# Performance work log

Measured on AMD Instinct MI355X. Metric: run time of the kernel, lower is better.

## Reference

```python
import jax, jax.numpy as jnp
import numpy as np

N = 30000   # nodes
E = 240000  # edges
G = 16      # graphs in batch
DIMS = [1, 256, 512, 1024]
OUT = 1024

def _xavier(key, fan_in, fan_out):
    lim = float(np.sqrt(6.0 / (fan_in + fan_out)))
    return jax.random.uniform(key, (fan_in, fan_out), minval=-lim, maxval=lim, dtype=jnp.float32)

def setup_inputs() -> dict:
    key = jax.random.key(0)
    ks = jax.random.split(key, 8)
    x = jax.random.normal(ks[0], (N, DIMS[0]), dtype=jnp.float32)
    edge_index = jax.random.randint(ks[1], (2, E), 0, N, dtype=jnp.int64)
    batch = jnp.sort(jax.random.randint(ks[2], (N,), 0, G, dtype=jnp.int64))
    W1 = _xavier(ks[3], DIMS[0], DIMS[1]); b1 = jnp.zeros((DIMS[1],), jnp.float32)
    W2 = _xavier(ks[4], DIMS[1], DIMS[2]); b2 = jnp.zeros((DIMS[2],), jnp.float32)
    W3 = _xavier(ks[5], DIMS[2], DIMS[3]); b3 = jnp.zeros((DIMS[3],), jnp.float32)
    Wo = _xavier(ks[6], DIMS[3], OUT);     bo = jnp.zeros((OUT,), jnp.float32)
    return {"x": x, "edge_index": edge_index, "batch": batch,
            "W1": W1, "b1": b1, "W2": W2, "b2": b2, "W3": W3, "b3": b3,
            "Wo": Wo, "bo": bo}

def reference(x, edge_index, batch, W1, b1, W2, b2, W3, b3, Wo, bo):
    n = x.shape[0]
    loops = jnp.arange(n)
    # GCNConv adds self-loops, then symmetric deg^-1/2 normalization
    src = jnp.concatenate([edge_index[0], loops])
    dst = jnp.concatenate([edge_index[1], loops])
    deg = jnp.zeros((n,), jnp.float32).at[dst].add(1.0)  # >=1 due to self-loops
    dis = jax.lax.rsqrt(deg)
    norm = (dis[src] * dis[dst])[:, None]  # [E+N, 1]

    def gcn(h, W, b):
        h = h @ W                                   # linear (no bias in lin)
        agg = jnp.zeros_like(h).at[dst].add(h[src] * norm)  # scatter-add messages
        return agg + b                              # GCNConv bias

    h = jax.nn.relu(gcn(x, W1, b1))
    h = jax.nn.relu(gcn(h, W2, b2))
    h = jax.nn.relu(gcn(h, W3, b3))
    # global mean pool over graphs
    sums = jnp.zeros((G, h.shape[1]), h.dtype).at[batch].add(h)
    cnt = jnp.zeros((G,), h.dtype).at[batch].add(1.0)
    pooled = sums / jnp.maximum(cnt, 1.0)[:, None]
    return pooled @ Wo + bo
```

## Files before the change

### kernel.cpp

```cpp
#include <hip/hip_runtime.h>
#include <hip/hip_bf16.h>
#include <stdint.h>

#define N_NODES 30000
#define E_EDGES 240000
#define NGRAPH  16
#define D1      256
#define D2      512
#define D3      1024
#define DOUT    1024
#define M_PAD   30720
#define NT_M    240
#define CAP     40

typedef unsigned short ushort_t;
typedef short short8 __attribute__((ext_vector_type(8)));
typedef float f32x4 __attribute__((ext_vector_type(4)));

__device__ __forceinline__ float bf2f(ushort_t u) {
    union { unsigned int i; float f; } v; v.i = ((unsigned int)u) << 16; return v.f;
}
__device__ __forceinline__ ushort_t f2bf(float x) {
    union { float f; unsigned int i; } v; v.f = x;
    unsigned int r = v.i + 0x7fffu + ((v.i >> 16) & 1u);
    return (ushort_t)(r >> 16);
}

__global__ void k_detect(const void* w1, const void* ei, int* flags) {
    int lane = threadIdx.x & 63;
    const ushort_t* h = (const ushort_t*)w1;
    float v = fabsf(bf2f(h[lane * 2]));
    unsigned long long badf = __ballot(!(v <= 0.25f));
    const int* e = (const int*)ei;
    unsigned long long badi = __ballot(e[lane * 2 + 1] != 0);
    if (threadIdx.x == 0) {
        flags[0] = (badf == 0ull) ? 1 : 0;
        flags[1] = (badi == 0ull) ? 1 : 0;
    }
}

__global__ void k_setup(const void* x, const void* batch, const void* w1, const void* b1,
                        const void* b2, const void* b3, const void* bo,
                        const void* W2, const void* W3,
                        float* xf, int* batch32, float* W1f, float* b1f, float* b2f,
                        float* b3f, float* bof, ushort_t* Wt2, ushort_t* Wt3,
                        int* slotcnt, float* pooled, float* pooled2, const int* flags) {
    int isbf = flags[0];
    int bid = blockIdx.x;
    int tid = threadIdx.x;
    if (bid < 492) {
        int i = bid * 256 + tid;
        if (i < 3072) {
            const void* src; float* dst; int idx;
            if      (i < 256)  { src = w1; dst = W1f; idx = i; }
            else if (i < 512)  { src = b1; dst = b1f; idx = i - 256; }
            else if (i < 1024) { src = b2; dst = b2f; idx = i - 512; }
            else if (i < 2048) { src = b3; dst = b3f; idx = i - 1024; }
            else               { src = bo; dst = bof; idx = i - 2048; }
            dst[idx] = isbf ? bf2f(((const ushort_t*)src)[idx]) : ((const float*)src)[idx];
        } else if (i < 33072) {
            int idx = i - 3072;
            xf[idx] = isbf ? bf2f(((const ushort_t*)x)[idx]) : ((const float*)x)[idx];
        } else if (i < 63072) {
            int idx = i - 33072;
            batch32[idx] = flags[1] ? (int)((const long long*)batch)[idx]
                                    : ((const int*)batch)[idx];
        } else if (i < 93072) {
            slotcnt[i - 63072] = 0;
        } else if (i < 109456) {
            pooled[i - 93072] = 0.0f;
        } else if (i < 125840) {
            pooled2[i - 109456] = 0.0f;
        }
    } else {
        __shared__ ushort_t tile[32][33];
        int tb = bid - 492;
        const void* in; ushort_t* out; int R, C, bx, by;
        if (tb < 128) { in = W2; out = Wt2; R = D1; C = D2; bx = tb & 15; by = tb >> 4; }
        else { tb -= 128; in = W3; out = Wt3; R = D2; C = D3; bx = tb & 31; by = tb >> 5; }
        int tx = tid & 31, ty = tid >> 5;
        int c0 = bx * 32, r0 = by * 32;
        for (int i = ty; i < 32; i += 8) {
            size_t idx = (size_t)(r0 + i) * C + c0 + tx;
            tile[i][tx] = isbf ? ((const ushort_t*)in)[idx] : f2bf(((const float*)in)[idx]);
        }
        __syncthreads();
        for (int i = ty; i < 32; i += 8) out[(size_t)(c0 + i) * R + r0 + tx] = tile[tx][i];
    }
}

__global__ void k_edge_count(const void* ei, int* slotcnt, int* slots, const int* flags) {
    int e = blockIdx.x * 256 + threadIdx.x;
    if (e >= E_EDGES) return;
    int s, d;
    if (flags[1]) {
        s = (int)((const long long*)ei)[e];
        d = (int)((const long long*)ei)[E_EDGES + e];
    } else {
        s = ((const int*)ei)[e];
        d = ((const int*)ei)[E_EDGES + e];
    }
    if ((unsigned)s >= N_NODES || (unsigned)d >= N_NODES) return;
    int pos = atomicAdd(&slotcnt[d], 1);
    if (pos < CAP) slots[d * CAP + pos] = s;
}

__global__ void k_node_cnt(const int* slotcnt, float* dis, const int* batch, float* cntg) {
    int b = blockIdx.x;
    if (b < 118) {
        int i = b * 256 + threadIdx.x;
        if (i < N_NODES) dis[i] = rsqrtf(1.0f + (float)slotcnt[i]);
    } else {
        int g = threadIdx.x;
        if (g >= NGRAPH) return;
        int lo0 = 0, hi0 = N_NODES;
        while (lo0 < hi0) { int m = (lo0 + hi0) >> 1; if (batch[m] < g) lo0 = m + 1; else hi0 = m; }
        int lo1 = lo0, hi1 = N_NODES;
        while (lo1 < hi1) { int m = (lo1 + hi1) >> 1; if (batch[m] < g + 1) lo1 = m + 1; else hi1 = m; }
        cntg[g] = (float)(lo1 - lo0);
    }
}

__global__ void k_s1(const float* xf, const float* dis, const int* slots,
                     const int* slotcnt, float* s1) {
    int d = blockIdx.x * 256 + threadIdx.x;
    if (d >= N_NODES) return;
    float di = dis[d];
    int cnt = slotcnt[d]; cnt = cnt < CAP ? cnt : CAP;
    float acc = xf[d] * di;
    for (int k = 0; k < cnt; k++) {
        int s = slots[d * CAP + k];
        acc += xf[s] * dis[s];
    }
    s1[d] = acc * di;
}

__global__ void k_agg1(const float* s1, const float* W1f, const float* b1f,
                       ushort_t* a2, const int* slots, const int* slotcnt, const float* dis) {
    int node = blockIdx.x * 4 + (threadIdx.x >> 6);
    int lane = threadIdx.x & 63;
    int c4 = lane * 4;
    float w[4], bb[4], a[4];
    #pragma unroll
    for (int j = 0; j < 4; j++) { w[j] = W1f[c4 + j]; bb[j] = b1f[c4 + j]; }
    float di = dis[node];
    int cnt = slotcnt[node]; cnt = cnt < CAP ? cnt : CAP;
    float sv = s1[node];
    float wsl = di * di;
    #pragma unroll
    for (int j = 0; j < 4; j++) a[j] = wsl * fmaxf(sv * w[j] + bb[j], 0.0f);
    for (int k = 0; k < cnt; k++) {
        int s = slots[node * CAP + k];
        float ss = s1[s];
        float wn = dis[s] * di;
        #pragma unroll
        for (int j = 0; j < 4; j++) a[j] += wn * fmaxf(ss * w[j] + bb[j], 0.0f);
    }
    uint2 o;
    o.x = (unsigned int)f2bf(a[0]) | ((unsigned int)f2bf(a[1]) << 16);
    o.y = (unsigned int)f2bf(a[2]) | ((unsigned int)f2bf(a[3]) << 16);
    *(uint2*)&a2[(size_t)node * D1 + c4] = o;
}

__global__ void k_agg2(const ushort_t* h, ushort_t* out, const int* slots,
                       const int* slotcnt, const float* dis) {
    int node = blockIdx.x * 4 + (threadIdx.x >> 6);
    int lane = threadIdx.x & 63;
    int c8 = lane * 8;
    float di = dis[node];
    int cnt = slotcnt[node]; cnt = cnt < CAP ? cnt : CAP;
    float w = di * di;
    const ushort_t* hp = h + c8;
    short8 p = *(const short8*)&hp[(size_t)node * D2];
    float a[8];
    #pragma unroll
    for (int j = 0; j < 8; j++) a[j] = w * bf2f((ushort_t)p[j]);
    if (cnt > 0) {
        int s0 = slots[node * CAP];
        short8 q0 = *(const short8*)&hp[(size_t)s0 * D2];
        float ws0 = dis[s0] * di;
        for (int k = 1; k < cnt; k++) {
            int s1i = slots[node * CAP + k];
            short8 q1 = *(const short8*)&hp[(size_t)s1i * D2];
            float ws1 = dis[s1i] * di;
            #pragma unroll
            for (int j = 0; j < 8; j++) a[j] += ws0 * bf2f((ushort_t)q0[j]);
            q0 = q1; ws0 = ws1;
        }
        #pragma unroll
        for (int j = 0; j < 8; j++) a[j] += ws0 * bf2f((ushort_t)q0[j]);
    }
    uint4 o;
    o.x = (unsigned int)f2bf(a[0]) | ((unsigned int)f2bf(a[1]) << 16);
    o.y = (unsigned int)f2bf(a[2]) | ((unsigned int)f2bf(a[3]) << 16);
    o.z = (unsigned int)f2bf(a[4]) | ((unsigned int)f2bf(a[5]) << 16);
    o.w = (unsigned int)f2bf(a[6]) | ((unsigned int)f2bf(a[7]) << 16);
    *(uint4*)&out[(size_t)node * D2 + c8] = o;
}

__global__ __launch_bounds__(256, 3) void k_gemm(const ushort_t* A, const ushort_t* Bt,
                                                 const float* bias, ushort_t* Cmat,
                                                 int K, int Ncols, int ntn) {
    __shared__ __align__(16) ushort_t As[2][128 * 32];
    __shared__ __align__(16) ushort_t Bs[2][128 * 32];
    int tid = threadIdx.x;
    int id = blockIdx.x;
    int xcd = id & 7, q = id >> 3;
    int rt = xcd * (NT_M / 8) + q / ntn;
    int ct = q % ntn;
    int bm0 = rt * 128, bn0 = ct * 128;
    int wave = tid >> 6, lane = tid & 63;
    int wm = (wave & 1) * 64, wn = (wave >> 1) * 64;
    int l15 = lane & 15, quad = lane >> 4;

    int m1 = tid >> 2, k1 = (tid & 3) << 3;
    int m2 = m1 + 64;
    int off1 = m1 * 32 + k1, off2 = m2 * 32 + k1;
    const ushort_t* pA1 = A + (size_t)(bm0 + m1) * K + k1;
    const ushort_t* pA2 = A + (size_t)(bm0 + m2) * K + k1;
    const ushort_t* pB1 = Bt + (size_t)(bn0 + m1) * K + k1;
    const ushort_t* pB2 = Bt + (size_t)(bn0 + m2) * K + k1;

    {
        uint4 la0 = *(const uint4*)pA1, la1 = *(const uint4*)pA2;
        uint4 lb0 = *(const uint4*)pB1, lb1 = *(const uint4*)pB2;
        *(uint4*)&As[0][off1] = la0; *(uint4*)&As[0][off2] = la1;
        *(uint4*)&Bs[0][off1] = lb0; *(uint4*)&Bs[0][off2] = lb1;
    }

    f32x4 acc[4][4];
    for (int a = 0; a < 4; a++)
        for (int b = 0; b < 4; b++)
            acc[a][b] = (f32x4){0.f, 0.f, 0.f, 0.f};

    int niter = K >> 5;
    for (int it = 0; it < niter; ++it) {
        __syncthreads();
        int ktn = (it + 1) << 5;
        uint4 na0, na1, nb0, nb1;
        if (ktn < K) {
            na0 = *(const uint4*)(pA1 + ktn); na1 = *(const uint4*)(pA2 + ktn);
            nb0 = *(const uint4*)(pB1 + ktn); nb1 = *(const uint4*)(pB2 + ktn);
        }
        int cb = it & 1;
        short8 af[4], bfr[4];
        for (int im = 0; im < 4; im++)
            af[im] = *(const short8*)&As[cb][(wm + im * 16 + l15) * 32 + quad * 8];
        for (int in = 0; in < 4; in++)
            bfr[in] = *(const short8*)&Bs[cb][(wn + in * 16 + l15) * 32 + quad * 8];
        for (int im = 0; im < 4; im++)
            for (int in = 0; in < 4; in++)
                acc[im][in] = __builtin_amdgcn_mfma_f32_16x16x32_bf16(af[im], bfr[in], acc[im][in], 0, 0, 0);
        if (ktn < K) {
            int wb = cb ^ 1;
            *(uint4*)&As[wb][off1] = na0; *(uint4*)&As[wb][off2] = na1;
            *(uint4*)&Bs[wb][off1] = nb0; *(uint4*)&Bs[wb][off2] = nb1;
        }
    }

    for (int im = 0; im < 4; im++) {
        int row = bm0 + wm + im * 16 + quad * 4;
        for (int in = 0; in < 4; in++) {
            int col = bn0 + wn + in * 16 + l15;
            float bv = bias[col];
            for (int r = 0; r < 4; r++) {
                float v = acc[im][in][r] + bv;
                v = v > 0.0f ? v : 0.0f;
                Cmat[(size_t)(row + r) * Ncols + col] = f2bf(v);
            }
        }
    }
}

__global__ __launch_bounds__(256, 3) void k_gemm_pool(const ushort_t* A, const ushort_t* Bt,
                                                      const float* bias, const int* batch,
                                                      float* pooled, int K, int ntn) {
    __shared__ __align__(16) ushort_t As[2][128 * 32];
    __shared__ __align__(16) ushort_t Bs[2][128 * 32];
    __shared__ float pl[NGRAPH * 128];
    __shared__ int gtile[128];
    int tid = threadIdx.x;
    int id = blockIdx.x;
    int xcd = id & 7, q = id >> 3;
    int rt = xcd * (NT_M / 8) + q / ntn;
    int ct = q % ntn;
    int bm0 = rt * 128, bn0 = ct * 128;
    int wave = tid >> 6, lane = tid & 63;
    int wm = (wave & 1) * 64, wn = (wave >> 1) * 64;
    int l15 = lane & 15, quad = lane >> 4;

    for (int i = tid; i < NGRAPH * 128; i += 256) pl[i] = 0.0f;
    if (tid < 128) {
        int r = bm0 + tid; if (r > N_NODES - 1) r = N_NODES - 1;
        int g = batch[r]; g = g < 0 ? 0 : (g > NGRAPH - 1 ? NGRAPH - 1 : g);
        gtile[tid] = g;
    }

    int m1 = tid >> 2, k1 = (tid & 3) << 3;
    int m2 = m1 + 64;
    int off1 = m1 * 32 + k1, off2 = m2 * 32 + k1;
    const ushort_t* pA1 = A + (size_t)(bm0 + m1) * K + k1;
    const ushort_t* pA2 = A + (size_t)(bm0 + m2) * K + k1;
    const ushort_t* pB1 = Bt + (size_t)(bn0 + m1) * K + k1;
    const ushort_t* pB2 = Bt + (size_t)(bn0 + m2) * K + k1;

    {
        uint4 la0 = *(const uint4*)pA1, la1 = *(const uint4*)pA2;
        uint4 lb0 = *(const uint4*)pB1, lb1 = *(const uint4*)pB2;
        *(uint4*)&As[0][off1] = la0; *(uint4*)&As[0][off2] = la1;
        *(uint4*)&Bs[0][off1] = lb0; *(uint4*)&Bs[0][off2] = lb1;
    }

    f32x4 acc[4][4];
    for (int a = 0; a < 4; a++)
        for (int b = 0; b < 4; b++)
            acc[a][b] = (f32x4){0.f, 0.f, 0.f, 0.f};

    int niter = K >> 5;
    for (int it = 0; it < niter; ++it) {
        __syncthreads();
        int ktn = (it + 1) << 5;
        uint4 na0, na1, nb0, nb1;
        if (ktn < K) {
            na0 = *(const uint4*)(pA1 + ktn); na1 = *(const uint4*)(pA2 + ktn);
            nb0 = *(const uint4*)(pB1 + ktn); nb1 = *(const uint4*)(pB2 + ktn);
        }
        int cb = it & 1;
        short8 af[4], bfr[4];
        for (int im = 0; im < 4; im++)
            af[im] = *(const short8*)&As[cb][(wm + im * 16 + l15) * 32 + quad * 8];
        for (int in = 0; in < 4; in++)
            bfr[in] = *(const short8*)&Bs[cb][(wn + in * 16 + l15) * 32 + quad * 8];
        for (int im = 0; im < 4; im++)
            for (int in = 0; in < 4; in++)
                acc[im][in] = __builtin_amdgcn_mfma_f32_16x16x32_bf16(af[im], bfr[in], acc[im][in], 0, 0, 0);
        if (ktn < K) {
            int wb = cb ^ 1;
            *(uint4*)&As[wb][off1] = na0; *(uint4*)&As[wb][off2] = na1;
            *(uint4*)&Bs[wb][off1] = nb0; *(uint4*)&Bs[wb][off2] = nb1;
        }
    }

    int gmin = gtile[0], gmax = gtile[127];
    if (gmin == gmax && bm0 + 127 < N_NODES) {
        float csum[4];
        #pragma unroll
        for (int in = 0; in < 4; in++) csum[in] = 0.0f;
        for (int im = 0; im < 4; im++) {
            #pragma unroll
            for (int in = 0; in < 4; in++) {
                float bv = bias[bn0 + wn + in * 16 + l15];
                #pragma unroll
                for (int r = 0; r < 4; r++)
                    csum[in] += fmaxf(acc[im][in][r] + bv, 0.0f);
            }
        }
        #pragma unroll
        for (int in = 0; in < 4; in++) {
            csum[in] += __shfl_xor(csum[in], 16);
            csum[in] += __shfl_xor(csum[in], 32);
        }
        if (quad == 0) {
            #pragma unroll
            for (int in = 0; in < 4; in++)
                atomicAdd(&pl[gmin * 128 + wn + in * 16 + l15], csum[in]);
        }
    } else {
        for (int im = 0; im < 4; im++) {
            int rl = wm + im * 16 + quad * 4;
            for (int in = 0; in < 4; in++) {
                int cl = wn + in * 16 + l15;
                float bv = bias[bn0 + cl];
                float vsum = 0.0f;
                int gprev = gtile[rl];
                for (int r = 0; r < 4; r++) {
                    int row = bm0 + rl + r;
                    float v = (row < N_NODES) ? fmaxf(acc[im][in][r] + bv, 0.0f) : 0.0f;
                    int g = gtile[rl + r];
                    if (g != gprev) {
                        atomicAdd(&pl[gprev * 128 + cl], vsum);
                        vsum = 0.0f; gprev = g;
                    }
                    vsum += v;
                }
                atomicAdd(&pl[gprev * 128 + cl], vsum);
            }
        }
    }
    __syncthreads();

    int span = (gmax - gmin + 1) * 128;
    for (int idx = tid; idx < span; idx += 256) {
        int g = gmin + (idx >> 7), cl = idx & 127;
        float v = pl[g * 128 + cl];
        if (v != 0.0f) atomicAdd(&pooled[g * DOUT + bn0 + cl], v);
    }
}

__global__ __launch_bounds__(256) void k_out_partial(const float* pooled, const void* Wo,
                                                     float* pooled2, const int* flags) {
    __shared__ float pl[NGRAPH * 32];
    int tid = threadIdx.x;
    int col = blockIdx.x * 256 + tid;
    int k0 = blockIdx.y * 32;
    for (int i = tid; i < NGRAPH * 32; i += 256) {
        int g = i >> 5, kk = i & 31;
        pl[i] = pooled[g * D3 + k0 + kk];
    }
    __syncthreads();
    int isbf = flags[0];
    float acc[NGRAPH];
    #pragma unroll
    for (int g = 0; g < NGRAPH; g++) acc[g] = 0.0f;
    #pragma unroll 4
    for (int kk = 0; kk < 32; kk++) {
        int k = k0 + kk;
        float wv = isbf ? bf2f(((const ushort_t*)Wo)[(size_t)k * DOUT + col])
                        : ((const float*)Wo)[(size_t)k * DOUT + col];
        #pragma unroll
        for (int g = 0; g < NGRAPH; g++)
            acc[g] += pl[g * 32 + kk] * wv;
    }
    #pragma unroll
    for (int g = 0; g < NGRAPH; g++)
        atomicAdd(&pooled2[g * DOUT + col], acc[g]);
}

__global__ void k_out_fin(const float* pooled2, const float* bof, const float* cntg,
                          void* out, const int* flags) {
    int i = blockIdx.x * 256 + threadIdx.x;
    int g = i >> 10, o = i & 1023;
    float c = cntg[g]; c = c > 1.0f ? c : 1.0f;
    float v = pooled2[i] / c + bof[o];
    if (flags[0]) ((ushort_t*)out)[i] = f2bf(v);
    else          ((float*)out)[i] = v;
}

extern "C" void kernel_launch(void* const* d_in, const int* in_sizes, int n_in,
                              void* d_out, int out_size, void* d_ws, size_t ws_size,
                              hipStream_t stream) {
    const void* x_raw  = d_in[0];
    const void* ei_raw = d_in[1];
    const void* b_raw  = d_in[2];
    const void* W1_raw = d_in[3];
    const void* b1_raw = d_in[4];
    const void* W2_raw = d_in[5];
    const void* b2_raw = d_in[6];
    const void* W3_raw = d_in[7];
    const void* b3_raw = d_in[8];
    const void* Wo_raw = d_in[9];
    const void* bo_raw = d_in[10];

    char* w = (char*)d_ws;
    size_t off = 0;
    auto alloc = [&](size_t b) { size_t o = off; off += (b + 255) & ~(size_t)255; return o; };
    int*   flags   = (int*)  (w + alloc(256));
    float* xf      = (float*)(w + alloc((size_t)N_NODES * 4));
    int*   batch32 = (int*)  (w + alloc((size_t)N_NODES * 4));
    float* W1f     = (float*)(w + alloc(D1 * 4));
    float* b1f     = (float*)(w + alloc(D1 * 4));
    float* b2f     = (float*)(w + alloc(D2 * 4));
    float* b3f     = (float*)(w + alloc(D3 * 4));
    float* bof     = (float*)(w + alloc(DOUT * 4));
    float* dis     = (float*)(w + alloc((size_t)N_NODES * 4));
    float* s1      = (float*)(w + alloc((size_t)N_NODES * 4));
    float* cntg    = (float*)(w + alloc(64));
    float* pooled  = (float*)(w + alloc((size_t)NGRAPH * DOUT * 4));
    float* pooled2 = (float*)(w + alloc((size_t)NGRAPH * DOUT * 4));
    int*   slotcnt = (int*)  (w + alloc((size_t)N_NODES * 4));
    int*   slots   = (int*)  (w + alloc((size_t)N_NODES * CAP * 4));
    ushort_t* Wt2  = (ushort_t*)(w + alloc((size_t)D2 * D1 * 2));
    ushort_t* Wt3  = (ushort_t*)(w + alloc((size_t)D3 * D2 * 2));
    ushort_t* slabA = (ushort_t*)(w + alloc((size_t)M_PAD * D2 * 2));
    ushort_t* a2 = slabA;
    ushort_t* a3 = slabA;
    ushort_t* h2   = (ushort_t*)(w + alloc((size_t)M_PAD * D2 * 2));

    int nb_e = (E_EDGES + 255) / 256;

    k_detect<<<1, 64, 0, stream>>>(W1_raw, ei_raw, flags);
    k_setup<<<1132, 256, 0, stream>>>(x_raw, b_raw, W1_raw, b1_raw, b2_raw, b3_raw, bo_raw,
                                      W2_raw, W3_raw, xf, batch32, W1f, b1f, b2f, b3f, bof,
                                      Wt2, Wt3, slotcnt, pooled, pooled2, flags);
    k_edge_count<<<nb_e, 256, 0, stream>>>(ei_raw, slotcnt, slots, flags);
    k_node_cnt<<<119, 256, 0, stream>>>(slotcnt, dis, batch32, cntg);
    k_s1<<<118, 256, 0, stream>>>(xf, dis, slots, slotcnt, s1);

    k_agg1<<<N_NODES / 4, 256, 0, stream>>>(s1, W1f, b1f, a2, slots, slotcnt, dis);
    k_gemm<<<NT_M * (D2 / 128), 256, 0, stream>>>(a2, Wt2, b2f, h2, D1, D2, D2 / 128);
    k_agg2<<<N_NODES / 4, 256, 0, stream>>>(h2, a3, slots, slotcnt, dis);
    k_gemm_pool<<<NT_M * (D3 / 128), 256, 0, stream>>>(a3, Wt3, b3f, batch32, pooled, D2, D3 / 128);

    k_out_partial<<<dim3(DOUT / 256, D3 / 32), 256, 0, stream>>>(pooled, Wo_raw, pooled2, flags);
    k_out_fin<<<NGRAPH * DOUT / 256, 256, 0, stream>>>(pooled2, bof, cntg, d_out, flags);
}
```

Baseline: 254.9 us.

## Double K-tile depth to 64 with padded LDS rows in GEMM kernels

Both GEMM kernels now stage 64-wide K tiles instead of 32, halving the number of barrier-separated iterations, and pad each LDS row to a stride of 72 elements to reduce bank conflicts on fragment reads. The pooling kernel reuses the A/B staging buffers for its partial-sum and graph-id scratch after the main loop, adding an extra barrier. Launch bounds drop from 3 to 2 blocks per CU to fit the larger shared memory footprint and extra prefetch registers, which lowers occupancy.

```diff
diff --git a/kernel.cpp b/kernel.cpp
--- a/kernel.cpp
+++ b/kernel.cpp
@@ -12,6 +12,7 @@
 #define M_PAD   30720
 #define NT_M    240
 #define CAP     40
+#define LSTR    72
 
 typedef unsigned short ushort_t;
 typedef short short8 __attribute__((ext_vector_type(8)));
@@ -198,11 +199,11 @@
     *(uint4*)&out[(size_t)node * D2 + c8] = o;
 }
 
-__global__ __launch_bounds__(256, 3) void k_gemm(const ushort_t* A, const ushort_t* Bt,
+__global__ __launch_bounds__(256, 2) void k_gemm(const ushort_t* A, const ushort_t* Bt,
                                                  const float* bias, ushort_t* Cmat,
                                                  int K, int Ncols, int ntn) {
-    __shared__ __align__(16) ushort_t As[2][128 * 32];
-    __shared__ __align__(16) ushort_t Bs[2][128 * 32];
+    __shared__ __align__(16) ushort_t As[2][128 * LSTR];
+    __shared__ __align__(16) ushort_t Bs[2][128 * LSTR];
     int tid = threadIdx.x;
     int id = blockIdx.x;
     int xcd = id & 7, q = id >> 3;
@@ -213,19 +214,19 @@
     int wm = (wave & 1) * 64, wn = (wave >> 1) * 64;
     int l15 = lane & 15, quad = lane >> 4;
 
-    int m1 = tid >> 2, k1 = (tid & 3) << 3;
-    int m2 = m1 + 64;
-    int off1 = m1 * 32 + k1, off2 = m2 * 32 + k1;
-    const ushort_t* pA1 = A + (size_t)(bm0 + m1) * K + k1;
-    const ushort_t* pA2 = A + (size_t)(bm0 + m2) * K + k1;
-    const ushort_t* pB1 = Bt + (size_t)(bn0 + m1) * K + k1;
-    const ushort_t* pB2 = Bt + (size_t)(bn0 + m2) * K + k1;
+    int srow = tid >> 1, skofs = (tid & 1) * 32;
+    int sofs = srow * LSTR + skofs;
+    const ushort_t* gA = A + (size_t)(bm0 + srow) * K + skofs;
+    const ushort_t* gB = Bt + (size_t)(bn0 + srow) * K + skofs;
 
     {
-        uint4 la0 = *(const uint4*)pA1, la1 = *(const uint4*)pA2;
-        uint4 lb0 = *(const uint4*)pB1, lb1 = *(const uint4*)pB2;
-        *(uint4*)&As[0][off1] = la0; *(uint4*)&As[0][off2] = la1;
-        *(uint4*)&Bs[0][off1] = lb0; *(uint4*)&Bs[0][off2] = lb1;
+        #pragma unroll
+        for (int j = 0; j < 4; j++) {
+            uint4 a = *(const uint4*)(gA + j * 8);
+            uint4 b = *(const uint4*)(gB + j * 8);
+            *(uint4*)&As[0][sofs + j * 8] = a;
+            *(uint4*)&Bs[0][sofs + j * 8] = b;
+        }
     }
 
     f32x4 acc[4][4];
@@ -233,28 +234,41 @@
         for (int b = 0; b < 4; b++)
             acc[a][b] = (f32x4){0.f, 0.f, 0.f, 0.f};
 
-    int niter = K >> 5;
+    int niter = K >> 6;
     for (int it = 0; it < niter; ++it) {
         __syncthreads();
-        int ktn = (it + 1) << 5;
-        uint4 na0, na1, nb0, nb1;
-        if (ktn < K) {
-            na0 = *(const uint4*)(pA1 + ktn); na1 = *(const uint4*)(pA2 + ktn);
-            nb0 = *(const uint4*)(pB1 + ktn); nb1 = *(const uint4*)(pB2 + ktn);
+        int kb = (it + 1) << 6;
+        uint4 na[4], nb[4];
+        if (kb < K) {
+            #pragma unroll
+            for (int j = 0; j < 4; j++) {
+                na[j] = *(const uint4*)(gA + kb + j * 8);
+                nb[j] = *(const uint4*)(gB + kb + j * 8);
+            }
         }
         int cb = it & 1;
-        short8 af[4], bfr[4];
-        for (int im = 0; im < 4; im++)
-            af[im] = *(const short8*)&As[cb][(wm + im * 16 + l15) * 32 + quad * 8];
-        for (int in = 0; in < 4; in++)
-            bfr[in] = *(const short8*)&Bs[cb][(wn + in * 16 + l15) * 32 + quad * 8];
-        for (int im = 0; im < 4; im++)
+        #pragma unroll
+        for (int h = 0; h < 2; h++) {
+            short8 af[4], bfr[4];
+            #pragma unroll
+            for (int im = 0; im < 4; im++)
+                af[im] = *(const short8*)&As[cb][(wm + im * 16 + l15) * LSTR + h * 32 + quad * 8];
+            #pragma unroll
             for (int in = 0; in < 4; in++)
-                acc[im][in] = __builtin_amdgcn_mfma_f32_16x16x32_bf16(af[im], bfr[in], acc[im][in], 0, 0, 0);
-        if (ktn < K) {
+                bfr[in] = *(const short8*)&Bs[cb][(wn + in * 16 + l15) * LSTR + h * 32 + quad * 8];
+            #pragma unroll
+            for (int im = 0; im < 4; im++)
+                #pragma unroll
+                for (int in = 0; in < 4; in++)
+                    acc[im][in] = __builtin_amdgcn_mfma_f32_16x16x32_bf16(af[im], bfr[in], acc[im][in], 0, 0, 0);
+        }
+        if (kb < K) {
             int wb = cb ^ 1;
-            *(uint4*)&As[wb][off1] = na0; *(uint4*)&As[wb][off2] = na1;
-            *(uint4*)&Bs[wb][off1] = nb0; *(uint4*)&Bs[wb][off2] = nb1;
+            #pragma unroll
+            for (int j = 0; j < 4; j++) {
+                *(uint4*)&As[wb][sofs + j * 8] = na[j];
+                *(uint4*)&Bs[wb][sofs + j * 8] = nb[j];
+            }
         }
     }
 
@@ -272,13 +286,11 @@
     }
 }
 
-__global__ __launch_bounds__(256, 3) void k_gemm_pool(const ushort_t* A, const ushort_t* Bt,
+__global__ __launch_bounds__(256, 2) void k_gemm_pool(const ushort_t* A, const ushort_t* Bt,
                                                       const float* bias, const int* batch,
                                                       float* pooled, int K, int ntn) {
-    __shared__ __align__(16) ushort_t As[2][128 * 32];
-    __shared__ __align__(16) ushort_t Bs[2][128 * 32];
-    __shared__ float pl[NGRAPH * 128];
-    __shared__ int gtile[128];
+    __shared__ __align__(16) ushort_t As[2][128 * LSTR];
+    __shared__ __align__(16) ushort_t Bs[2][128 * LSTR];
     int tid = threadIdx.x;
     int id = blockIdx.x;
     int xcd = id & 7, q = id >> 3;
@@ -289,57 +301,74 @@
     int wm = (wave & 1) * 64, wn = (wave >> 1) * 64;
     int l15 = lane & 15, quad = lane >> 4;
 
+    int srow = tid >> 1, skofs = (tid & 1) * 32;
+    int sofs = srow * LSTR + skofs;
+    const ushort_t* gA = A + (size_t)(bm0 + srow) * K + skofs;
+    const ushort_t* gB = Bt + (size_t)(bn0 + srow) * K + skofs;
+
+    {
+        #pragma unroll
+        for (int j = 0; j < 4; j++) {
+            uint4 a = *(const uint4*)(gA + j * 8);
+            uint4 b = *(const uint4*)(gB + j * 8);
+            *(uint4*)&As[0][sofs + j * 8] = a;
+            *(uint4*)&Bs[0][sofs + j * 8] = b;
+        }
+    }
+
+    f32x4 acc[4][4];
+    for (int a = 0; a < 4; a++)
+        for (int b = 0; b < 4; b++)
+            acc[a][b] = (f32x4){0.f, 0.f, 0.f, 0.f};
+
+    int niter = K >> 6;
+    for (int it = 0; it < niter; ++it) {
+        __syncthreads();
+        int kb = (it + 1) << 6;
+        uint4 na[4], nb[4];
+        if (kb < K) {
+            #pragma unroll
+            for (int j = 0; j < 4; j++) {
+                na[j] = *(const uint4*)(gA + kb + j * 8);
+                nb[j] = *(const uint4*)(gB + kb + j * 8);
+            }
+        }
+        int cb = it & 1;
+        #pragma unroll
+        for (int h = 0; h < 2; h++) {
+            short8 af[4], bfr[4];
+            #pragma unroll
+            for (int im = 0; im < 4; im++)
+                af[im] = *(const short8*)&As[cb][(wm + im * 16 + l15) * LSTR + h * 32 + quad * 8];
+            #pragma unroll
+            for (int in = 0; in < 4; in++)
+                bfr[in] = *(const short8*)&Bs[cb][(wn + in * 16 + l15) * LSTR + h * 32 + quad * 8];
+            #pragma unroll
+            for (int im = 0; im < 4; im++)
+                #pragma unroll
+                for (int in = 0; in < 4; in++)
+                    acc[im][in] = __builtin_amdgcn_mfma_f32_16x16x32_bf16(af[im], bfr[in], acc[im][in], 0, 0, 0);
+        }
+        if (kb < K) {
+            int wb = cb ^ 1;
+            #pragma unroll
+            for (int j = 0; j < 4; j++) {
+                *(uint4*)&As[wb][sofs + j * 8] = na[j];
+                *(uint4*)&Bs[wb][sofs + j * 8] = nb[j];
+            }
+        }
+    }
+
+    __syncthreads();
+    float* pl = (float*)&As[0][0];
+    int* gtile = (int*)&Bs[0][0];
     for (int i = tid; i < NGRAPH * 128; i += 256) pl[i] = 0.0f;
     if (tid < 128) {
         int r = bm0 + tid; if (r > N_NODES - 1) r = N_NODES - 1;
         int g = batch[r]; g = g < 0 ? 0 : (g > NGRAPH - 1 ? NGRAPH - 1 : g);
         gtile[tid] = g;
     }
-
-    int m1 = tid >> 2, k1 = (tid & 3) << 3;
-    int m2 = m1 + 64;
-    int off1 = m1 * 32 + k1, off2 = m2 * 32 + k1;
-    const ushort_t* pA1 = A + (size_t)(bm0 + m1) * K + k1;
-    const ushort_t* pA2 = A + (size_t)(bm0 + m2) * K + k1;
-    const ushort_t* pB1 = Bt + (size_t)(bn0 + m1) * K + k1;
-    const ushort_t* pB2 = Bt + (size_t)(bn0 + m2) * K + k1;
-
-    {
-        uint4 la0 = *(const uint4*)pA1, la1 = *(const uint4*)pA2;
-        uint4 lb0 = *(const uint4*)pB1, lb1 = *(const uint4*)pB2;
-        *(uint4*)&As[0][off1] = la0; *(uint4*)&As[0][off2] = la1;
-        *(uint4*)&Bs[0][off1] = lb0; *(uint4*)&Bs[0][off2] = lb1;
-    }
-
-    f32x4 acc[4][4];
-    for (int a = 0; a < 4; a++)
-        for (int b = 0; b < 4; b++)
-            acc[a][b] = (f32x4){0.f, 0.f, 0.f, 0.f};
-
-    int niter = K >> 5;
-    for (int it = 0; it < niter; ++it) {
-        __syncthreads();
-        int ktn = (it + 1) << 5;
-        uint4 na0, na1, nb0, nb1;
-        if (ktn < K) {
-            na0 = *(const uint4*)(pA1 + ktn); na1 = *(const uint4*)(pA2 + ktn);
-            nb0 = *(const uint4*)(pB1 + ktn); nb1 = *(const uint4*)(pB2 + ktn);
-        }
-        int cb = it & 1;
-        short8 af[4], bfr[4];
-        for (int im = 0; im < 4; im++)
-            af[im] = *(const short8*)&As[cb][(wm + im * 16 + l15) * 32 + quad * 8];
-        for (int in = 0; in < 4; in++)
-            bfr[in] = *(const short8*)&Bs[cb][(wn + in * 16 + l15) * 32 + quad * 8];
-        for (int im = 0; im < 4; im++)
-            for (int in = 0; in < 4; in++)
-                acc[im][in] = __builtin_amdgcn_mfma_f32_16x16x32_bf16(af[im], bfr[in], acc[im][in], 0, 0, 0);
-        if (ktn < K) {
-            int wb = cb ^ 1;
-            *(uint4*)&As[wb][off1] = na0; *(uint4*)&As[wb][off2] = na1;
-            *(uint4*)&Bs[wb][off1] = nb0; *(uint4*)&Bs[wb][off2] = nb1;
-        }
-    }
+    __syncthreads();
 
     int gmin = gtile[0], gmax = gtile[127];
     if (gmin == gmax && bm0 + 127 < N_NODES) {
```

Measured after the change: 364.2 us. +42.9%, slower.
